# Kernel optimization log

Hardware: AMD Instinct MI355X
Metric: run time of the kernel (lower is better)

Reference implementation:

```python
import jax, jax.numpy as jnp
import numpy as np

S, B, V, E, H, C = 512, 64, 50000, 300, 256, 5


def setup_inputs() -> dict:
    key = jax.random.key(0)
    ks = jax.random.split(key, 8)
    return {
        "inputs": jax.random.randint(ks[0], (S, B), 0, V, dtype=jnp.int64),
        "emb": jax.random.normal(ks[1], (V, E), dtype=jnp.float32),
        # small weight scale to keep tanh out of saturation (matches typical init scale)
        "W_ih": jax.random.normal(ks[2], (H, E), dtype=jnp.float32) * 0.05,
        "W_hh": jax.random.normal(ks[3], (H, H), dtype=jnp.float32) * 0.05,
        "b_ih": jax.random.normal(ks[4], (H,), dtype=jnp.float32) * 0.05,
        "b_hh": jax.random.normal(ks[5], (H,), dtype=jnp.float32) * 0.05,
        "W_out": jax.random.normal(ks[6], (C, H), dtype=jnp.float32) * 0.05,
        "b_out": jax.random.normal(ks[7], (C,), dtype=jnp.float32) * 0.05,
    }


def reference(inputs, emb, W_ih, W_hh, b_ih, b_hh, W_out, b_out):
    # embedding lookup: (S, B, E)
    x = emb[inputs]
    # precompute input-to-hidden projection for all timesteps: (S, B, H)
    xW = jnp.einsum("sbe,he->sbh", x, W_ih) + b_ih

    def step(h, xw_t):
        h_new = jnp.tanh(xw_t + h @ W_hh.T + b_hh)
        return h_new, h_new

    h0 = jnp.zeros((inputs.shape[1], W_hh.shape[0]), dtype=x.dtype)
    _, rnn_out = jax.lax.scan(step, h0, xW)  # (S, B, H)

    logits = jnp.einsum("sbh,ch->sbc", rnn_out, W_out) + b_out  # (S, B, C)
    summed = logits.sum(axis=0)  # (B, C)
    return jax.nn.log_softmax(summed, axis=1)
```

## Files before the change

### kernel.cpp

```cpp
#include <hip/hip_runtime.h>
#include <stdint.h>

#define S_ 512
#define B_ 64
#define V_ 50000
#define E_ 300
#define H_ 256
#define C_ 5

typedef _Float16 h8_t __attribute__((ext_vector_type(8)));
typedef float f32x4 __attribute__((ext_vector_type(4)));

__device__ __forceinline__ float fast_tanh(float x) {
    float e = __builtin_amdgcn_exp2f(x * 2.88539008177793f);
    return fmaf(-2.0f, __builtin_amdgcn_rcpf(e + 1.0f), 1.0f);
}

__global__ void wb_prep_kernel(const float* __restrict__ W_ih,
                               uint4* __restrict__ WB) {
    int g = blockIdx.x * 256 + threadIdx.x;
    if (g >= 16 * 10 * 64) return;
    int l = g & 63;
    int ks = (g >> 6) % 10;
    int nt = g / 640;
    int h = nt * 16 + (l & 15);
    int e0 = ks * 32 + (l >> 4) * 8;
    h8_t v;
#pragma unroll
    for (int j = 0; j < 8; ++j) {
        int e = e0 + j;
        v[j] = (e < E_) ? (_Float16)W_ih[(size_t)h * E_ + e] : (_Float16)0.0f;
    }
    WB[g] = __builtin_bit_cast(uint4, v);
}

__global__ __launch_bounds__(512, 2) void xw_kernel(
    const int* __restrict__ idx, const float* __restrict__ emb,
    const uint4* __restrict__ WB, const float* __restrict__ b_ih,
    const float* __restrict__ b_hh, float* __restrict__ xw) {
    __shared__ uint4 Afrag[4 * 10 * 64];
    const int tid = threadIdx.x;
    const int w = tid >> 6;
    const int l = tid & 63;
    const int n = l & 15;
    const int hi = l >> 4;
    const int base = blockIdx.x * 64;

    for (int cc = tid; cc < 64 * 40; cc += 512) {
        int m = cc / 40;
        int c = cc - m * 40;
        int ks = c >> 2;
        int hic = c & 3;
        const float* src = emb + (size_t)idx[base + m] * E_ + 8 * c;
        h8_t v;
        if (c < 37) {
            float4 f0 = *(const float4*)src;
            float4 f1 = *(const float4*)(src + 4);
            v[0] = (_Float16)f0.x; v[1] = (_Float16)f0.y;
            v[2] = (_Float16)f0.z; v[3] = (_Float16)f0.w;
            v[4] = (_Float16)f1.x; v[5] = (_Float16)f1.y;
            v[6] = (_Float16)f1.z; v[7] = (_Float16)f1.w;
        } else if (c == 37) {
            float4 f0 = *(const float4*)src;
            v[0] = (_Float16)f0.x; v[1] = (_Float16)f0.y;
            v[2] = (_Float16)f0.z; v[3] = (_Float16)f0.w;
            v[4] = (_Float16)0.0f; v[5] = (_Float16)0.0f;
            v[6] = (_Float16)0.0f; v[7] = (_Float16)0.0f;
        } else {
            v = (h8_t)(_Float16)0.0f;
        }
        int fl = (hic << 4) | (m & 15);
        int mt = m >> 4;
        Afrag[(mt * 10 + ks) * 64 + fl] = __builtin_bit_cast(uint4, v);
    }
    __syncthreads();

    float bias0 = b_ih[w * 32 + n] + b_hh[w * 32 + n];
    float bias1 = b_ih[w * 32 + 16 + n] + b_hh[w * 32 + 16 + n];
    f32x4 c[4][2];
#pragma unroll
    for (int mt = 0; mt < 4; ++mt) {
        c[mt][0] = (f32x4)bias0;
        c[mt][1] = (f32x4)bias1;
    }

    const uint4* wb0 = WB + ((2 * w) * 10) * 64 + l;
    const uint4* wb1 = WB + ((2 * w + 1) * 10) * 64 + l;
#pragma unroll
    for (int ks = 0; ks < 10; ++ks) {
        h8_t b0 = __builtin_bit_cast(h8_t, wb0[ks * 64]);
        h8_t b1 = __builtin_bit_cast(h8_t, wb1[ks * 64]);
#pragma unroll
        for (int mt = 0; mt < 4; ++mt) {
            h8_t a = __builtin_bit_cast(h8_t, Afrag[(mt * 10 + ks) * 64 + l]);
            c[mt][0] = __builtin_amdgcn_mfma_f32_16x16x32_f16(a, b0, c[mt][0],
                                                              0, 0, 0);
            c[mt][1] = __builtin_amdgcn_mfma_f32_16x16x32_f16(a, b1, c[mt][1],
                                                              0, 0, 0);
        }
    }

#pragma unroll
    for (int mt = 0; mt < 4; ++mt)
#pragma unroll
        for (int q = 0; q < 2; ++q) {
            float* op =
                xw + (size_t)(base + mt * 16 + hi * 4) * H_ + w * 32 + q * 16 + n;
#pragma unroll
            for (int r = 0; r < 4; ++r) op[(size_t)r * H_] = c[mt][q][r];
        }
}

__global__ __launch_bounds__(512, 2) void rnn_kernel(
    const float* __restrict__ xw, const float* __restrict__ W_hh,
    float* __restrict__ hsum_out) {
    const int tid = threadIdx.x;
    const int w = tid >> 6;
    const int l = tid & 63;
    const int n = l & 15;
    const int hi = l >> 4;
    const int col = n & 7;
    const int sel = n >> 3;
    const int bbase = blockIdx.x * 8;
    const int rowbase = w * 32;

    __shared__ __attribute__((aligned(16))) unsigned char Hl[2][4096];
    char* lds = (char*)Hl;

    h8_t a[2][8];
#pragma unroll
    for (int mt = 0; mt < 2; ++mt) {
        const float* wr = W_hh + (size_t)(rowbase + mt * 16 + n) * H_;
#pragma unroll
        for (int ks = 0; ks < 8; ++ks) {
            const float* wp = wr + ks * 32 + hi * 8;
            float4 f0 = *(const float4*)wp;
            float4 f1 = *(const float4*)(wp + 4);
            h8_t v;
            v[0] = (_Float16)f0.x; v[1] = (_Float16)f0.y;
            v[2] = (_Float16)f0.z; v[3] = (_Float16)f0.w;
            v[4] = (_Float16)f1.x; v[5] = (_Float16)f1.y;
            v[6] = (_Float16)f1.z; v[7] = (_Float16)f1.w;
            a[mt][ks] = v;
        }
    }

    const int wboff =
        (w * 4 + sel * 2 + (hi >> 1)) * 128 + col * 16 + (hi & 1) * 8;
    const int rdbase = hi * 128 + col * 16;

    for (int t = tid; t < 1024; t += 512) ((unsigned int*)Hl)[t] = 0u;

    f32x4 hs = (f32x4)0.0f;

    const float* xwl = xw + (size_t)(bbase + col) * H_ + rowbase + hi * 4;
    f32x4 cv[4][2];
    cv[0][0] = *(const f32x4*)(xwl);
    cv[0][1] = *(const f32x4*)(xwl + 16);
    cv[1][0] = *(const f32x4*)(xwl + 16384);
    cv[1][1] = *(const f32x4*)(xwl + 16384 + 16);
    __syncthreads();

#define STEP(CUR, I, SBASE)                                                    \
    {                                                                          \
        int sp = (SBASE) + 2;                                                  \
        if (sp > S_ - 1) sp = S_ - 1;                                          \
        cv[(I + 2) & 3][0] = *(const f32x4*)(xwl + (size_t)sp * 16384);        \
        cv[(I + 2) & 3][1] = *(const f32x4*)(xwl + (size_t)sp * 16384 + 16);   \
        h8_t bf[8];                                                            \
        _Pragma("unroll") for (int ks = 0; ks < 8; ++ks)                       \
            bf[ks] = *(const h8_t*)(lds + (CUR)*4096 + rdbase + ks * 512);     \
        _Pragma("unroll") for (int ks = 0; ks < 8; ++ks) {                     \
            cv[I][0] = __builtin_amdgcn_mfma_f32_16x16x32_f16(                 \
                a[0][ks], bf[ks], cv[I][0], 0, 0, 0);                          \
            cv[I][1] = __builtin_amdgcn_mfma_f32_16x16x32_f16(                 \
                a[1][ks], bf[ks], cv[I][1], 0, 0, 0);                          \
        }                                                                      \
        {                                                                      \
            f32x4 sv = (sel == 0) ? cv[I][0] : cv[I][1];                       \
            float h0 = fast_tanh(sv[0]);                                       \
            float h1 = fast_tanh(sv[1]);                                       \
            float h2 = fast_tanh(sv[2]);                                       \
            float h3 = fast_tanh(sv[3]);                                       \
            hs[0] += h0; hs[1] += h1; hs[2] += h2; hs[3] += h3;                \
            uint2 pk;                                                          \
            pk.x = __builtin_bit_cast(unsigned int,                            \
                                      __builtin_amdgcn_cvt_pkrtz(h0, h1));     \
            pk.y = __builtin_bit_cast(unsigned int,                            \
                                      __builtin_amdgcn_cvt_pkrtz(h2, h3));     \
            *(uint2*)(lds + ((CUR) ^ 1) * 4096 + wboff) = pk;                  \
        }                                                                      \
        asm volatile("s_waitcnt lgkmcnt(0)" ::: "memory");                     \
        __builtin_amdgcn_s_barrier();                                          \
    }

    for (int s = 0; s < S_; s += 4) {
        STEP(0, 0, s)
        STEP(1, 1, s + 1)
        STEP(0, 2, s + 2)
        STEP(1, 3, s + 3)
    }
#undef STEP

    {
        float4 o;
        o.x = hs[0]; o.y = hs[1]; o.z = hs[2]; o.w = hs[3];
        *(float4*)(hsum_out + (size_t)(bbase + col) * H_ + rowbase + sel * 16 +
                   hi * 4) = o;
    }
}

__global__ void out_kernel(const float* __restrict__ hsum,
                           const float* __restrict__ W_out,
                           const float* __restrict__ b_out,
                           float* __restrict__ out) {
    int b = threadIdx.x;
    if (b >= B_) return;
    float logits[C_];
#pragma unroll
    for (int c = 0; c < C_; ++c) {
        float acc = 0.0f;
        for (int k = 0; k < H_; ++k)
            acc = fmaf(hsum[b * H_ + k], W_out[c * H_ + k], acc);
        logits[c] = acc + (float)S_ * b_out[c];
    }
    float m = logits[0];
#pragma unroll
    for (int c = 1; c < C_; ++c) m = fmaxf(m, logits[c]);
    float sum = 0.0f;
#pragma unroll
    for (int c = 0; c < C_; ++c) sum += expf(logits[c] - m);
    float lse = logf(sum);
#pragma unroll
    for (int c = 0; c < C_; ++c) out[b * C_ + c] = logits[c] - m - lse;
}

extern "C" void kernel_launch(void* const* d_in, const int* in_sizes, int n_in,
                              void* d_out, int out_size, void* d_ws,
                              size_t ws_size, hipStream_t stream) {
    const int* idx = (const int*)d_in[0];
    const float* emb = (const float*)d_in[1];
    const float* W_ih = (const float*)d_in[2];
    const float* W_hh = (const float*)d_in[3];
    const float* b_ih = (const float*)d_in[4];
    const float* b_hh = (const float*)d_in[5];
    const float* W_out = (const float*)d_in[6];
    const float* b_out = (const float*)d_in[7];
    float* out = (float*)d_out;

    float* ws = (float*)d_ws;
    uint4* WB = (uint4*)ws;
    float* xw = ws + 40960;
    float* hsum = xw + (size_t)S_ * B_ * H_;

    hipLaunchKernelGGL(wb_prep_kernel, dim3(40), dim3(256), 0, stream, W_ih,
                       WB);
    hipLaunchKernelGGL(xw_kernel, dim3((S_ * B_) / 64), dim3(512), 0, stream,
                       idx, emb, WB, b_ih, b_hh, xw);
    hipLaunchKernelGGL(rnn_kernel, dim3(8), dim3(512), 0, stream, xw, W_hh,
                       hsum);
    hipLaunchKernelGGL(out_kernel, dim3(1), dim3(64), 0, stream, hsum, W_out,
                       b_out, out);
}
```

Baseline: 281.4 us.

## Split RNN recurrence over 16 blocks with 4 batch columns each

Each RNN block now handles 4 batch columns instead of 8, so the grid doubles to 16 blocks and the LDS hidden-state buffers shrink by half. The tanh and LDS writes per lane drop from 4 to 2 elements, which shortens the serial per-step critical path. Each block still loads the full W_hh into registers and runs the same MFMA count on a half-empty 16-wide tile, so tensor-core utilisation per block falls.

```diff
diff --git a/kernel.cpp b/kernel.cpp
--- a/kernel.cpp
+++ b/kernel.cpp
@@ -119,12 +119,12 @@
     const int l = tid & 63;
     const int n = l & 15;
     const int hi = l >> 4;
-    const int col = n & 7;
-    const int sel = n >> 3;
-    const int bbase = blockIdx.x * 8;
+    const int col = n & 3;
+    const int d = n >> 2;
+    const int bbase = blockIdx.x * 4;
     const int rowbase = w * 32;
 
-    __shared__ __attribute__((aligned(16))) unsigned char Hl[2][4096];
+    __shared__ __attribute__((aligned(16))) unsigned char Hl[2][2048];
     char* lds = (char*)Hl;
 
     h8_t a[2][8];
@@ -145,13 +145,17 @@
         }
     }
 
-    const int wboff =
-        (w * 4 + sel * 2 + (hi >> 1)) * 128 + col * 16 + (hi & 1) * 8;
-    const int rdbase = hi * 128 + col * 16;
-
-    for (int t = tid; t < 1024; t += 512) ((unsigned int*)Hl)[t] = 0u;
-
-    f32x4 hs = (f32x4)0.0f;
+    const int t_ = d >> 1;
+    const int p_ = d & 1;
+    const int k0 = rowbase + t_ * 16 + hi * 4 + 2 * p_;
+    const int wboff = (k0 >> 3) * 64 + col * 16 + (k0 & 7) * 2;
+    const int rdbase = hi * 64 + col * 16;
+
+    if (tid < 512) ((unsigned int*)Hl)[tid] = 0u;
+
+    float2 hs;
+    hs.x = 0.0f;
+    hs.y = 0.0f;
 
     const float* xwl = xw + (size_t)(bbase + col) * H_ + rowbase + hi * 4;
     f32x4 cv[4][2];
@@ -169,7 +173,7 @@
         cv[(I + 2) & 3][1] = *(const f32x4*)(xwl + (size_t)sp * 16384 + 16);   \
         h8_t bf[8];                                                            \
         _Pragma("unroll") for (int ks = 0; ks < 8; ++ks)                       \
-            bf[ks] = *(const h8_t*)(lds + (CUR)*4096 + rdbase + ks * 512);     \
+            bf[ks] = *(const h8_t*)(lds + (CUR)*2048 + rdbase + ks * 256);     \
         _Pragma("unroll") for (int ks = 0; ks < 8; ++ks) {                     \
             cv[I][0] = __builtin_amdgcn_mfma_f32_16x16x32_f16(                 \
                 a[0][ks], bf[ks], cv[I][0], 0, 0, 0);                          \
@@ -177,18 +181,16 @@
                 a[1][ks], bf[ks], cv[I][1], 0, 0, 0);                          \
         }                                                                      \
         {                                                                      \
-            f32x4 sv = (sel == 0) ? cv[I][0] : cv[I][1];                       \
-            float h0 = fast_tanh(sv[0]);                                       \
-            float h1 = fast_tanh(sv[1]);                                       \
-            float h2 = fast_tanh(sv[2]);                                       \
-            float h3 = fast_tanh(sv[3]);                                       \
-            hs[0] += h0; hs[1] += h1; hs[2] += h2; hs[3] += h3;                \
-            uint2 pk;                                                          \
-            pk.x = __builtin_bit_cast(unsigned int,                            \
-                                      __builtin_amdgcn_cvt_pkrtz(h0, h1));     \
-            pk.y = __builtin_bit_cast(unsigned int,                            \
-                                      __builtin_amdgcn_cvt_pkrtz(h2, h3));     \
-            *(uint2*)(lds + ((CUR) ^ 1) * 4096 + wboff) = pk;                  \
+            f32x4 sv = (t_ == 0) ? cv[I][0] : cv[I][1];                        \
+            float e0 = (p_ == 0) ? sv[0] : sv[2];                              \
+            float e1 = (p_ == 0) ? sv[1] : sv[3];                              \
+            float h0 = fast_tanh(e0);                                          \
+            float h1 = fast_tanh(e1);                                          \
+            hs.x += h0;                                                        \
+            hs.y += h1;                                                        \
+            unsigned int pk = __builtin_bit_cast(                              \
+                unsigned int, __builtin_amdgcn_cvt_pkrtz(h0, h1));             \
+            *(unsigned int*)(lds + ((CUR) ^ 1) * 2048 + wboff) = pk;           \
         }                                                                      \
         asm volatile("s_waitcnt lgkmcnt(0)" ::: "memory");                     \
         __builtin_amdgcn_s_barrier();                                          \
@@ -203,10 +205,10 @@
 #undef STEP
 
     {
-        float4 o;
-        o.x = hs[0]; o.y = hs[1]; o.z = hs[2]; o.w = hs[3];
-        *(float4*)(hsum_out + (size_t)(bbase + col) * H_ + rowbase + sel * 16 +
-                   hi * 4) = o;
+        float2 o;
+        o.x = hs.x;
+        o.y = hs.y;
+        *(float2*)(hsum_out + (size_t)(bbase + col) * H_ + k0) = o;
     }
 }
 
@@ -257,7 +259,7 @@
                        WB);
     hipLaunchKernelGGL(xw_kernel, dim3((S_ * B_) / 64), dim3(512), 0, stream,
                        idx, emb, WB, b_ih, b_hh, xw);
-    hipLaunchKernelGGL(rnn_kernel, dim3(8), dim3(512), 0, stream, xw, W_hh,
+    hipLaunchKernelGGL(rnn_kernel, dim3(16), dim3(512), 0, stream, xw, W_hh,
                        hsum);
     hipLaunchKernelGGL(out_kernel, dim3(1), dim3(64), 0, stream, hsum, W_out,
                        b_out, out);
```

Result: no change. 276.9 us (-1.6%).

## Fuse input projection and recurrence into one kernel with counter-based overlap

Applied to the files above, without the earlier changes.

Merges the xw projection kernel and the RNN recurrence kernel into a single launch. Blocks 0-7 run the recurrence and blocks 8+ compute xw tiles. Producer blocks bump per-64-timestep global counters, and the recurrent blocks spin-wait on the matching counter before prefetching those timesteps. This lets the serial recurrence start while later projections are still being computed, hiding the projection phase and one launch gap. The cost is a spin-wait dependency that assumes the recurrent blocks and producers are co-resident, plus an extra memset launch.

```diff
diff --git a/kernel.cpp b/kernel.cpp
--- a/kernel.cpp
+++ b/kernel.cpp
@@ -14,6 +14,14 @@
 __device__ __forceinline__ float fast_tanh(float x) {
     float e = __builtin_amdgcn_exp2f(x * 2.88539008177793f);
     return fmaf(-2.0f, __builtin_amdgcn_rcpf(e + 1.0f), 1.0f);
+}
+
+__device__ __forceinline__ void wait_group(volatile unsigned* gcnt, int grp) {
+    while (__hip_atomic_load((const unsigned*)&gcnt[grp], __ATOMIC_RELAXED,
+                             __HIP_MEMORY_SCOPE_AGENT) != 64u) {
+        __builtin_amdgcn_s_sleep(16);
+    }
+    __builtin_amdgcn_fence(__ATOMIC_ACQUIRE, "agent");
 }
 
 __global__ void wb_prep_kernel(const float* __restrict__ W_ih,
@@ -34,87 +42,97 @@
     WB[g] = __builtin_bit_cast(uint4, v);
 }
 
-__global__ __launch_bounds__(512, 2) void xw_kernel(
+__global__ __launch_bounds__(512, 2) void fused_kernel(
     const int* __restrict__ idx, const float* __restrict__ emb,
     const uint4* __restrict__ WB, const float* __restrict__ b_ih,
-    const float* __restrict__ b_hh, float* __restrict__ xw) {
-    __shared__ uint4 Afrag[4 * 10 * 64];
+    const float* __restrict__ b_hh, float* __restrict__ xw,
+    const float* __restrict__ W_hh, float* __restrict__ hsum_out,
+    unsigned* __restrict__ gcnt) {
+    __shared__ __attribute__((aligned(16))) unsigned char smem[40960];
     const int tid = threadIdx.x;
-    const int w = tid >> 6;
-    const int l = tid & 63;
-    const int n = l & 15;
-    const int hi = l >> 4;
-    const int base = blockIdx.x * 64;
-
-    for (int cc = tid; cc < 64 * 40; cc += 512) {
-        int m = cc / 40;
-        int c = cc - m * 40;
-        int ks = c >> 2;
-        int hic = c & 3;
-        const float* src = emb + (size_t)idx[base + m] * E_ + 8 * c;
-        h8_t v;
-        if (c < 37) {
-            float4 f0 = *(const float4*)src;
-            float4 f1 = *(const float4*)(src + 4);
-            v[0] = (_Float16)f0.x; v[1] = (_Float16)f0.y;
-            v[2] = (_Float16)f0.z; v[3] = (_Float16)f0.w;
-            v[4] = (_Float16)f1.x; v[5] = (_Float16)f1.y;
-            v[6] = (_Float16)f1.z; v[7] = (_Float16)f1.w;
-        } else if (c == 37) {
-            float4 f0 = *(const float4*)src;
-            v[0] = (_Float16)f0.x; v[1] = (_Float16)f0.y;
-            v[2] = (_Float16)f0.z; v[3] = (_Float16)f0.w;
-            v[4] = (_Float16)0.0f; v[5] = (_Float16)0.0f;
-            v[6] = (_Float16)0.0f; v[7] = (_Float16)0.0f;
-        } else {
-            v = (h8_t)(_Float16)0.0f;
-        }
-        int fl = (hic << 4) | (m & 15);
-        int mt = m >> 4;
-        Afrag[(mt * 10 + ks) * 64 + fl] = __builtin_bit_cast(uint4, v);
-    }
-    __syncthreads();
-
-    float bias0 = b_ih[w * 32 + n] + b_hh[w * 32 + n];
-    float bias1 = b_ih[w * 32 + 16 + n] + b_hh[w * 32 + 16 + n];
-    f32x4 c[4][2];
-#pragma unroll
-    for (int mt = 0; mt < 4; ++mt) {
-        c[mt][0] = (f32x4)bias0;
-        c[mt][1] = (f32x4)bias1;
-    }
-
-    const uint4* wb0 = WB + ((2 * w) * 10) * 64 + l;
-    const uint4* wb1 = WB + ((2 * w + 1) * 10) * 64 + l;
-#pragma unroll
-    for (int ks = 0; ks < 10; ++ks) {
-        h8_t b0 = __builtin_bit_cast(h8_t, wb0[ks * 64]);
-        h8_t b1 = __builtin_bit_cast(h8_t, wb1[ks * 64]);
+
+    if (blockIdx.x >= 8) {
+        const int g = blockIdx.x - 8;
+        uint4* Afrag = (uint4*)smem;
+        const int w = tid >> 6;
+        const int l = tid & 63;
+        const int n = l & 15;
+        const int hi = l >> 4;
+        const int base = g * 64;
+
+        for (int cc = tid; cc < 64 * 40; cc += 512) {
+            int m = cc / 40;
+            int c = cc - m * 40;
+            int ks = c >> 2;
+            int hic = c & 3;
+            const float* src = emb + (size_t)idx[base + m] * E_ + 8 * c;
+            h8_t v;
+            if (c < 37) {
+                float4 f0 = *(const float4*)src;
+                float4 f1 = *(const float4*)(src + 4);
+                v[0] = (_Float16)f0.x; v[1] = (_Float16)f0.y;
+                v[2] = (_Float16)f0.z; v[3] = (_Float16)f0.w;
+                v[4] = (_Float16)f1.x; v[5] = (_Float16)f1.y;
+                v[6] = (_Float16)f1.z; v[7] = (_Float16)f1.w;
+            } else if (c == 37) {
+                float4 f0 = *(const float4*)src;
+                v[0] = (_Float16)f0.x; v[1] = (_Float16)f0.y;
+                v[2] = (_Float16)f0.z; v[3] = (_Float16)f0.w;
+                v[4] = (_Float16)0.0f; v[5] = (_Float16)0.0f;
+                v[6] = (_Float16)0.0f; v[7] = (_Float16)0.0f;
+            } else {
+                v = (h8_t)(_Float16)0.0f;
+            }
+            int fl = (hic << 4) | (m & 15);
+            int mt = m >> 4;
+            Afrag[(mt * 10 + ks) * 64 + fl] = __builtin_bit_cast(uint4, v);
+        }
+        __syncthreads();
+
+        float bias0 = b_ih[w * 32 + n] + b_hh[w * 32 + n];
+        float bias1 = b_ih[w * 32 + 16 + n] + b_hh[w * 32 + 16 + n];
+        f32x4 c[4][2];
 #pragma unroll
         for (int mt = 0; mt < 4; ++mt) {
-            h8_t a = __builtin_bit_cast(h8_t, Afrag[(mt * 10 + ks) * 64 + l]);
-            c[mt][0] = __builtin_amdgcn_mfma_f32_16x16x32_f16(a, b0, c[mt][0],
-                                                              0, 0, 0);
-            c[mt][1] = __builtin_amdgcn_mfma_f32_16x16x32_f16(a, b1, c[mt][1],
-                                                              0, 0, 0);
-        }
-    }
-
-#pragma unroll
-    for (int mt = 0; mt < 4; ++mt)
-#pragma unroll
-        for (int q = 0; q < 2; ++q) {
-            float* op =
-                xw + (size_t)(base + mt * 16 + hi * 4) * H_ + w * 32 + q * 16 + n;
-#pragma unroll
-            for (int r = 0; r < 4; ++r) op[(size_t)r * H_] = c[mt][q][r];
-        }
-}
-
-__global__ __launch_bounds__(512, 2) void rnn_kernel(
-    const float* __restrict__ xw, const float* __restrict__ W_hh,
-    float* __restrict__ hsum_out) {
-    const int tid = threadIdx.x;
+            c[mt][0] = (f32x4)bias0;
+            c[mt][1] = (f32x4)bias1;
+        }
+
+        const uint4* wb0 = WB + ((2 * w) * 10) * 64 + l;
+        const uint4* wb1 = WB + ((2 * w + 1) * 10) * 64 + l;
+#pragma unroll
+        for (int ks = 0; ks < 10; ++ks) {
+            h8_t b0 = __builtin_bit_cast(h8_t, wb0[ks * 64]);
+            h8_t b1 = __builtin_bit_cast(h8_t, wb1[ks * 64]);
+#pragma unroll
+            for (int mt = 0; mt < 4; ++mt) {
+                h8_t a =
+                    __builtin_bit_cast(h8_t, Afrag[(mt * 10 + ks) * 64 + l]);
+                c[mt][0] = __builtin_amdgcn_mfma_f32_16x16x32_f16(
+                    a, b0, c[mt][0], 0, 0, 0);
+                c[mt][1] = __builtin_amdgcn_mfma_f32_16x16x32_f16(
+                    a, b1, c[mt][1], 0, 0, 0);
+            }
+        }
+
+#pragma unroll
+        for (int mt = 0; mt < 4; ++mt)
+#pragma unroll
+            for (int q = 0; q < 2; ++q) {
+                float* op = xw + (size_t)(base + mt * 16 + hi * 4) * H_ +
+                            w * 32 + q * 16 + n;
+#pragma unroll
+                for (int r = 0; r < 4; ++r) op[(size_t)r * H_] = c[mt][q][r];
+            }
+
+        __syncthreads();
+        if (tid == 0) {
+            __threadfence();
+            atomicAdd(&gcnt[g >> 6], 1u);
+        }
+        return;
+    }
+
     const int w = tid >> 6;
     const int l = tid & 63;
     const int n = l & 15;
@@ -124,8 +142,7 @@
     const int bbase = blockIdx.x * 8;
     const int rowbase = w * 32;
 
-    __shared__ __attribute__((aligned(16))) unsigned char Hl[2][4096];
-    char* lds = (char*)Hl;
+    char* lds = (char*)smem;
 
     h8_t a[2][8];
 #pragma unroll
@@ -149,9 +166,11 @@
         (w * 4 + sel * 2 + (hi >> 1)) * 128 + col * 16 + (hi & 1) * 8;
     const int rdbase = hi * 128 + col * 16;
 
-    for (int t = tid; t < 1024; t += 512) ((unsigned int*)Hl)[t] = 0u;
+    for (int t = tid; t < 1024; t += 512) ((unsigned int*)lds)[t] = 0u;
 
     f32x4 hs = (f32x4)0.0f;
+
+    wait_group(gcnt, 0);
 
     const float* xwl = xw + (size_t)(bbase + col) * H_ + rowbase + hi * 4;
     f32x4 cv[4][2];
@@ -164,6 +183,7 @@
 #define STEP(CUR, I, SBASE)                                                    \
     {                                                                          \
         int sp = (SBASE) + 2;                                                  \
+        if (sp < S_ && (sp & 63) == 0) wait_group(gcnt, sp >> 6);              \
         if (sp > S_ - 1) sp = S_ - 1;                                          \
         cv[(I + 2) & 3][0] = *(const f32x4*)(xwl + (size_t)sp * 16384);        \
         cv[(I + 2) & 3][1] = *(const f32x4*)(xwl + (size_t)sp * 16384 + 16);   \
@@ -252,13 +272,13 @@
     uint4* WB = (uint4*)ws;
     float* xw = ws + 40960;
     float* hsum = xw + (size_t)S_ * B_ * H_;
-
+    unsigned* gcnt = (unsigned*)(hsum + B_ * H_);
+
+    hipMemsetAsync(gcnt, 0, 8 * sizeof(unsigned), stream);
     hipLaunchKernelGGL(wb_prep_kernel, dim3(40), dim3(256), 0, stream, W_ih,
                        WB);
-    hipLaunchKernelGGL(xw_kernel, dim3((S_ * B_) / 64), dim3(512), 0, stream,
-                       idx, emb, WB, b_ih, b_hh, xw);
-    hipLaunchKernelGGL(rnn_kernel, dim3(8), dim3(512), 0, stream, xw, W_hh,
-                       hsum);
+    hipLaunchKernelGGL(fused_kernel, dim3(520), dim3(512), 0, stream, idx, emb,
+                       WB, b_ih, b_hh, xw, W_hh, hsum, gcnt);
     hipLaunchKernelGGL(out_kernel, dim3(1), dim3(64), 0, stream, hsum, W_out,
                        b_out, out);
 }
```

Measured after the change: 301.1 us. 7.0% more time.
